# Optimization experiments

Hardware: AMD Instinct MI355X
Metric: run time of the kernel (lower is better)

Reference implementation:

```python
import jax, jax.numpy as jnp
import numpy as np
from jax import lax

B, T, D, LD, K = 128, 1024, 256, 512, 128
RD = LD + K  # 640 residual-LSTM width
PAD = 15     # (31 - 1) // 2 'same' padding for the LSA location conv


def _gru(x, h, wih, whh, bih, bhh):
    # torch.nn.GRUCell semantics, gate order [r, z, n]
    gi = x @ wih.T + bih
    gh = h @ whh.T + bhh
    ir, iz, inn = jnp.split(gi, 3, axis=-1)
    hr, hz, hn = jnp.split(gh, 3, axis=-1)
    r = jax.nn.sigmoid(ir + hr)
    z = jax.nn.sigmoid(iz + hz)
    n = jnp.tanh(inn + r * hn)
    return (1.0 - z) * n + z * h


def _lstm(x, h, c, wih, whh, bih, bhh):
    # torch.nn.LSTMCell semantics, gate order [i, f, g, o]
    g = x @ wih.T + bih + h @ whh.T + bhh
    i, f, gg, o = jnp.split(g, 4, axis=-1)
    c2 = jax.nn.sigmoid(f) * c + jax.nn.sigmoid(i) * jnp.tanh(gg)
    h2 = jax.nn.sigmoid(o) * jnp.tanh(c2)
    return h2, c2


def _forward(encoder_seq, encoder_seq_proj, prenet_in, attn_hidden, rnn1_h, rnn1_c,
             rnn2_h, rnn2_c, res_h, res_c, context_vec, cumulative, attn_prev,
             fc1_w, fc1_b, fc2_w, fc2_b, gru_wih, gru_whh, gru_bih, gru_bhh,
             conv_w, L_w, L_b, W_w, W_b, v_w, ri_w, ri_b,
             r1_wih, r1_whh, r1_bih, r1_bhh, r2_wih, r2_whh, r2_bih, r2_bhh,
             res_wih, res_whh, res_bih, res_bhh, stop_w, stop_b):
    # PreNet (dropout p = 0 in Decoder.__init__, so pure tanh-MLP)
    p = jnp.tanh(prenet_in @ fc1_w.T + fc1_b)
    prenet_out = jnp.tanh(p @ fc2_w.T + fc2_b)                     # [B, D//2]
    # Attention GRU
    attn_in = jnp.concatenate([context_vec, prenet_out], axis=-1)  # [B, D + D//2]
    attn_h = _gru(attn_in, attn_hidden, gru_wih, gru_whh, gru_bih, gru_bhh)  # [B, D]
    # LSA location-sensitive attention (cumulative/attn_prev are zeros at t=0)
    pq = (attn_h @ W_w.T + W_b)[:, None, :]                        # [B, 1, D]
    loc = jnp.stack([cumulative, attn_prev], axis=1)               # [B, 2, T]
    conv_out = lax.conv_general_dilated(loc, conv_w, (1,), [(PAD, PAD)],
                                        dimension_numbers=('NCH', 'OIH', 'NCH'))  # [B, 32, T]
    ploc = jnp.swapaxes(conv_out, 1, 2) @ L_w.T + L_b              # [B, T, D]
    u = jnp.squeeze(jnp.tanh(pq + encoder_seq_proj + ploc) @ v_w.T, -1)  # [B, T]
    sig = jax.nn.sigmoid(u)
    scores = sig / jnp.sum(sig, axis=1, keepdims=True)             # [B, T]
    cum_new = cumulative + scores
    context = jnp.einsum('bt,btd->bd', scores, encoder_seq)        # [B, D]
    # rnn_input projection + two residual LSTM cells (eval: no zoneout)
    x = jnp.concatenate([context, attn_h], axis=1) @ ri_w.T + ri_b  # [B, LD]
    h1, c1 = _lstm(x, rnn1_h, rnn1_c, r1_wih, r1_whh, r1_bih, r1_bhh)
    x = x + h1
    h2, c2 = _lstm(x, rnn2_h, rnn2_c, r2_wih, r2_whh, r2_bih, r2_bhh)
    x = x + h2
    # 4-layer residual LSTM stack on [prenet_in, x]
    res_x = jnp.concatenate([prenet_in, x], axis=1)                # [B, RD]
    hs, cs = [], []
    for i in range(4):
        hi, ci = _lstm(res_x, res_h[i], res_c[i], res_wih[i], res_whh[i], res_bih[i], res_bhh[i])
        res_x = res_x + hi
        hs.append(hi)
        cs.append(ci)
    cond = res_x                                                   # cond_features [B, RD]
    stop = jax.nn.sigmoid(cond @ stop_w.T + stop_b)                # [B, 1]
    return (cond, stop, scores, attn_h, h1, c1, h2, c2,
            jnp.stack(hs), jnp.stack(cs), context, cum_new)


def setup_inputs() -> dict:
    keys = iter(jax.random.split(jax.random.key(0), 64))
    nxt = lambda: next(keys)
    rn = lambda s: jax.random.normal(nxt(), s, jnp.float32)
    wp = lambda s: rn(s) * 0.02
    return {
        'encoder_seq': rn((B, T, D)),
        'encoder_seq_proj': rn((B, T, D)),
        'prenet_in': rn((B, K)),
        'attn_hidden': rn((B, D)),
        'rnn1_h': rn((B, LD)), 'rnn1_c': rn((B, LD)),
        'rnn2_h': rn((B, LD)), 'rnn2_c': rn((B, LD)),
        'res_h': rn((4, B, RD)), 'res_c': rn((4, B, RD)),
        'context_vec': rn((B, D)),
        'cumulative': jnp.zeros((B, T), jnp.float32),
        'attn_prev': jnp.zeros((B, T), jnp.float32),
        'fc1_w': wp((256, K)), 'fc1_b': jnp.zeros((256,), jnp.float32),
        'fc2_w': wp((D // 2, 256)), 'fc2_b': jnp.zeros((D // 2,), jnp.float32),
        'gru_wih': wp((3 * D, D + D // 2)), 'gru_whh': wp((3 * D, D)),
        'gru_bih': jnp.zeros((3 * D,), jnp.float32), 'gru_bhh': jnp.zeros((3 * D,), jnp.float32),
        'conv_w': wp((32, 2, 31)),
        'L_w': wp((D, 32)), 'L_b': jnp.zeros((D,), jnp.float32),
        'W_w': wp((D, D)), 'W_b': jnp.zeros((D,), jnp.float32),
        'v_w': wp((1, D)),
        'ri_w': wp((LD, 2 * D)), 'ri_b': jnp.zeros((LD,), jnp.float32),
        'r1_wih': wp((4 * LD, LD)), 'r1_whh': wp((4 * LD, LD)),
        'r1_bih': jnp.zeros((4 * LD,), jnp.float32), 'r1_bhh': jnp.zeros((4 * LD,), jnp.float32),
        'r2_wih': wp((4 * LD, LD)), 'r2_whh': wp((4 * LD, LD)),
        'r2_bih': jnp.zeros((4 * LD,), jnp.float32), 'r2_bhh': jnp.zeros((4 * LD,), jnp.float32),
        'res_wih': wp((4, 4 * RD, RD)), 'res_whh': wp((4, 4 * RD, RD)),
        'res_bih': jnp.zeros((4, 4 * RD), jnp.float32), 'res_bhh': jnp.zeros((4, 4 * RD), jnp.float32),
        'stop_w': wp((1, RD)), 'stop_b': jnp.zeros((1,), jnp.float32),
    }


def reference(encoder_seq, encoder_seq_proj, prenet_in, attn_hidden, rnn1_h, rnn1_c,
              rnn2_h, rnn2_c, res_h, res_c, context_vec, cumulative, attn_prev,
              fc1_w, fc1_b, fc2_w, fc2_b, gru_wih, gru_whh, gru_bih, gru_bhh,
              conv_w, L_w, L_b, W_w, W_b, v_w, ri_w, ri_b,
              r1_wih, r1_whh, r1_bih, r1_bhh, r2_wih, r2_whh, r2_bih, r2_bhh,
              res_wih, res_whh, res_bih, res_bhh, stop_w, stop_b):
    return _forward(encoder_seq, encoder_seq_proj, prenet_in, attn_hidden, rnn1_h, rnn1_c,
                    rnn2_h, rnn2_c, res_h, res_c, context_vec, cumulative, attn_prev,
                    fc1_w, fc1_b, fc2_w, fc2_b, gru_wih, gru_whh, gru_bih, gru_bhh,
                    conv_w, L_w, L_b, W_w, W_b, v_w, ri_w, ri_b,
                    r1_wih, r1_whh, r1_bih, r1_bhh, r2_wih, r2_whh, r2_bih, r2_bhh,
                    res_wih, res_whh, res_bih, res_bhh, stop_w, stop_b)
```

## Files before the change

### kernel.cpp

```cpp
#include <hip/hip_runtime.h>

#define DEV __device__ __forceinline__

typedef __attribute__((ext_vector_type(8))) short short8;
typedef __attribute__((ext_vector_type(4))) float f32x4;

DEV float fast_rcp(float x) { return __builtin_amdgcn_rcpf(x); }
DEV float sigm(float x) { return fast_rcp(1.0f + __expf(-x)); }
DEV float tanhf_fast(float x) { return 1.0f - 2.0f * fast_rcp(1.0f + __expf(2.0f * x)); }

DEV short f2bf(float f) {
    unsigned u = __float_as_uint(f);
    unsigned r = (u + 0x7FFFu + ((u >> 16) & 1u)) >> 16;
    return (short)r;
}
DEV float bf2f(short h) {
    return __uint_as_float(((unsigned)(unsigned short)h) << 16);
}
DEV void split1(float f, short& h, short& l) {
    h = f2bf(f);
    l = f2bf(f - bf2f(h));
}

__global__ __launch_bounds__(256) void convert_w_kernel(
    const float* __restrict__ p0, const float* __restrict__ p1,
    const float* __restrict__ p2, const float* __restrict__ p3,
    const float* __restrict__ p4, const float* __restrict__ p5,
    const float* __restrict__ p6, const float* __restrict__ p7,
    const float* __restrict__ p8, const float* __restrict__ p9,
    const float* __restrict__ p10, const float* __restrict__ p11,
    short* __restrict__ hi, short* __restrict__ lo)
{
    const int c1 = 8192, c2 = 16384, c3 = 90112, c4 = 139264, c5 = 155648,
              c6 = 221184, c7 = 483328, c8 = 745472, c9 = 1007616,
              c10 = 1269760, c11 = 2908160, total = 4546560;
    for (int v = blockIdx.x * 256 + threadIdx.x; v < total; v += gridDim.x * 256) {
        const float* s = p0; int base = 0;
        if (v >= c1)  { s = p1;  base = c1; }
        if (v >= c2)  { s = p2;  base = c2; }
        if (v >= c3)  { s = p3;  base = c3; }
        if (v >= c4)  { s = p4;  base = c4; }
        if (v >= c5)  { s = p5;  base = c5; }
        if (v >= c6)  { s = p6;  base = c6; }
        if (v >= c7)  { s = p7;  base = c7; }
        if (v >= c8)  { s = p8;  base = c8; }
        if (v >= c9)  { s = p9;  base = c9; }
        if (v >= c10) { s = p10; base = c10; }
        if (v >= c11) { s = p11; base = c11; }
        float4 f = ((const float4*)s)[v - base];
        short4 h, l;
        split1(f.x, h.x, l.x);
        split1(f.y, h.y, l.y);
        split1(f.z, h.z, l.z);
        split1(f.w, h.w, l.w);
        ((short4*)hi)[v] = h;
        ((short4*)lo)[v] = l;
    }
}

__global__ __launch_bounds__(256) void gemm_mfma_kernel(
    const float* __restrict__ A1, int K1,
    const short* __restrict__ W1hi, const short* __restrict__ W1lo, int ldw1,
    const float* __restrict__ A2, int K2,
    const short* __restrict__ W2hi, const short* __restrict__ W2lo, int ldw2,
    float* __restrict__ Cp, int N, int KS, int KC)
{
    const int tid = threadIdx.x;
    const int chunk = blockIdx.x % KS;
    const int n0 = (blockIdx.x / KS) * 32;
    const int kbeg = chunk * KC;
    const int w = tid >> 6, lane = tid & 63;
    const int q = lane >> 4, r = lane & 15;
    const int m_base = w * 32;

    f32x4 acc[2][2];
#pragma unroll
    for (int mt = 0; mt < 2; ++mt)
#pragma unroll
        for (int nt = 0; nt < 2; ++nt)
            acc[mt][nt] = (f32x4){0.f, 0.f, 0.f, 0.f};

    auto load_frag = [&](int kg, float4 (&a)[2][2], short8 (&bh)[2], short8 (&bl)[2]) {
        const float* A; const short *Wh, *Wl; int lda, ldw, kc;
        if (kg < K1) { A = A1; Wh = W1hi; Wl = W1lo; lda = K1; ldw = ldw1; kc = kg; }
        else         { A = A2; Wh = W2hi; Wl = W2lo; lda = K2; ldw = ldw2; kc = kg - K1; }
#pragma unroll
        for (int mt = 0; mt < 2; ++mt) {
            const float* ap = A + (size_t)(m_base + mt * 16 + r) * lda + kc + q * 8;
            a[mt][0] = *(const float4*)ap;
            a[mt][1] = *(const float4*)(ap + 4);
        }
#pragma unroll
        for (int nt = 0; nt < 2; ++nt) {
            size_t off = (size_t)(n0 + nt * 16 + r) * ldw + kc + q * 8;
            bh[nt] = *(const short8*)(Wh + off);
            bl[nt] = *(const short8*)(Wl + off);
        }
    };

    auto compute = [&](const float4 (&a)[2][2], const short8 (&bh)[2], const short8 (&bl)[2]) {
#pragma unroll
        for (int mt = 0; mt < 2; ++mt) {
            float fv[8] = {a[mt][0].x, a[mt][0].y, a[mt][0].z, a[mt][0].w,
                           a[mt][1].x, a[mt][1].y, a[mt][1].z, a[mt][1].w};
            short8 ah, al;
#pragma unroll
            for (int j = 0; j < 8; ++j) {
                short h, l;
                split1(fv[j], h, l);
                ah[j] = h; al[j] = l;
            }
#pragma unroll
            for (int nt = 0; nt < 2; ++nt) {
                acc[mt][nt] = __builtin_amdgcn_mfma_f32_16x16x32_bf16(ah, bh[nt], acc[mt][nt], 0, 0, 0);
                acc[mt][nt] = __builtin_amdgcn_mfma_f32_16x16x32_bf16(al, bh[nt], acc[mt][nt], 0, 0, 0);
                acc[mt][nt] = __builtin_amdgcn_mfma_f32_16x16x32_bf16(ah, bl[nt], acc[mt][nt], 0, 0, 0);
            }
        }
    };

    float4 a0[2][2], a1[2][2];
    short8 bh0[2], bl0[2], bh1[2], bl1[2];
    const int nsteps = KC >> 5;

    load_frag(kbeg, a0, bh0, bl0);
    for (int s = 0; s + 1 < nsteps; ++s) {
        if (s & 1) { load_frag(kbeg + (s + 1) * 32, a0, bh0, bl0); compute(a1, bh1, bl1); }
        else       { load_frag(kbeg + (s + 1) * 32, a1, bh1, bl1); compute(a0, bh0, bl0); }
    }
    if ((nsteps - 1) & 1) compute(a1, bh1, bl1);
    else                  compute(a0, bh0, bl0);

    float* Co = Cp + (size_t)chunk * 128 * N;
#pragma unroll
    for (int mt = 0; mt < 2; ++mt)
#pragma unroll
        for (int nt = 0; nt < 2; ++nt)
#pragma unroll
            for (int i = 0; i < 4; ++i)
                Co[(size_t)(m_base + mt * 16 + q * 4 + i) * N + n0 + nt * 16 + r] = acc[mt][nt][i];
}

__global__ void reduce_act_kernel(const float* __restrict__ p, int KS, int MN,
                                  const float* __restrict__ b,
                                  float* __restrict__ out, int N, int act)
{
    int idx = blockIdx.x * 256 + threadIdx.x;
    if (idx >= MN) return;
    int n = idx % N;
    float v = b ? b[n] : 0.f;
    for (int s = 0; s < KS; ++s) v += p[(size_t)s * MN + idx];
    if (act) v = tanhf_fast(v);
    out[idx] = v;
}

__global__ void gru_gate_kernel(const float* __restrict__ gi_p, int KSi,
                                const float* __restrict__ gh_p, int KSh,
                                const float* __restrict__ bih, const float* __restrict__ bhh,
                                const float* __restrict__ h, float* __restrict__ out)
{
    const size_t MN = 128 * 768;
    int m = blockIdx.x, d = threadIdx.x;
    size_t base = (size_t)m * 768 + d;
    float ir = bih[d], iz = bih[256 + d], in = bih[512 + d];
    for (int s = 0; s < KSi; ++s) {
        const float* p = gi_p + s * MN + base;
        ir += p[0]; iz += p[256]; in += p[512];
    }
    float hr = bhh[d], hz = bhh[256 + d], hn = bhh[512 + d];
    for (int s = 0; s < KSh; ++s) {
        const float* p = gh_p + s * MN + base;
        hr += p[0]; hz += p[256]; hn += p[512];
    }
    float r = sigm(ir + hr);
    float z = sigm(iz + hz);
    float n = tanhf_fast(in + r * hn);
    out[m * 256 + d] = (1.f - z) * n + z * h[m * 256 + d];
}

__global__ void lstm_gate_kernel(const float* __restrict__ gp, int KS,
                                 const float* __restrict__ bih, const float* __restrict__ bhh,
                                 const float* __restrict__ c_in,
                                 float* __restrict__ h_out, float* __restrict__ c_out,
                                 float* __restrict__ xacc, int H)
{
    int d = blockIdx.x * 256 + threadIdx.x;
    int m = blockIdx.y;
    if (d >= H) return;
    const size_t MN = (size_t)128 * 4 * H;
    size_t base = (size_t)m * 4 * H + d;
    float iv = bih[d] + bhh[d];
    float fv = bih[H + d] + bhh[H + d];
    float gv = bih[2 * H + d] + bhh[2 * H + d];
    float ov = bih[3 * H + d] + bhh[3 * H + d];
    for (int s = 0; s < KS; ++s) {
        const float* p = gp + s * MN + base;
        iv += p[0]; fv += p[H]; gv += p[2 * H]; ov += p[3 * H];
    }
    float c2 = sigm(fv) * c_in[m * H + d] + sigm(iv) * tanhf_fast(gv);
    float h2 = sigm(ov) * tanhf_fast(c2);
    h_out[m * H + d] = h2;
    c_out[m * H + d] = c2;
    if (xacc) xacc[m * H + d] += h2;
}

__global__ void lw_bf16_kernel(const float* __restrict__ Lw, short* __restrict__ LwBf)
{
    int i = blockIdx.x * 256 + threadIdx.x;
    LwBf[i] = f2bf(Lw[i]);
}

__global__ __launch_bounds__(256) void attn_u_kernel(
    const float* __restrict__ esp, const float* __restrict__ pq,
    const short* __restrict__ LwBf, const float* __restrict__ Lb,
    const float* __restrict__ vw, const float* __restrict__ cw,
    const float* __restrict__ cum, const float* __restrict__ prev,
    float* __restrict__ sig_out)
{
    const int b = blockIdx.x >> 4;
    const int t0 = (blockIdx.x & 15) << 6;
    const int tid = threadIdx.x;

    __shared__ float cum_s[94], prev_s[94];
    __shared__ float cw_s[2][32][33];
    __shared__ short conv_bf[64 * 32];
    __shared__ short lw_bf[256 * 32];
    __shared__ float pq_s[256], vw_s[256];

    if (tid < 94) {
        int ti = t0 - 15 + tid;
        cum_s[tid] = (ti >= 0 && ti < 1024) ? cum[b * 1024 + ti] : 0.f;
    } else if (tid >= 128 && tid < 222) {
        int i = tid - 128;
        int ti = t0 - 15 + i;
        prev_s[i] = (ti >= 0 && ti < 1024) ? prev[b * 1024 + ti] : 0.f;
    }
    for (int i = tid; i < 2048; i += 256) {
        int which = i >> 10, c = (i >> 5) & 31, k = i & 31;
        cw_s[which][c][k] = (k < 31) ? cw[(c * 2 + which) * 31 + k] : 0.f;
    }
    {
        const int4* src = (const int4*)LwBf;
        int4* dst = (int4*)lw_bf;
#pragma unroll
        for (int k = 0; k < 4; ++k) dst[tid + k * 256] = src[tid + k * 256];
    }
    pq_s[tid] = pq[b * 256 + tid] + Lb[tid];
    vw_s[tid] = vw[tid];
    __syncthreads();

    {
        int c = tid & 31, t8 = (tid >> 5) << 3;
        float a[8] = {0.f, 0.f, 0.f, 0.f, 0.f, 0.f, 0.f, 0.f};
        for (int k = 0; k < 31; ++k) {
            float w0 = cw_s[0][c][k], w1 = cw_s[1][c][k];
#pragma unroll
            for (int j = 0; j < 8; ++j)
                a[j] += w0 * cum_s[t8 + j + k] + w1 * prev_s[t8 + j + k];
        }
#pragma unroll
        for (int j = 0; j < 8; ++j) conv_bf[(t8 + j) * 32 + c] = f2bf(a[j]);
    }
    __syncthreads();

    const int lane = tid & 63, w = tid >> 6;
    const int q = lane >> 4, c16 = lane & 15;
    const int myt = t0 + w * 16 + c16;

    short8 bfrag = *(const short8*)&conv_bf[(w * 16 + c16) * 32 + q * 8];
    const float* er = esp + ((size_t)(b * 1024 + myt) << 8);

    float s = 0.f;
#pragma unroll
    for (int dt = 0; dt < 16; ++dt) {
        short8 afrag = *(const short8*)&lw_bf[(dt * 16 + c16) * 32 + q * 8];
        f32x4 acc = {0.f, 0.f, 0.f, 0.f};
        acc = __builtin_amdgcn_mfma_f32_16x16x32_bf16(afrag, bfrag, acc, 0, 0, 0);
        const int d0 = dt * 16 + q * 4;
        float4 e   = *(const float4*)(er + d0);
        float4 pqv = *(const float4*)&pq_s[d0];
        float4 vwv = *(const float4*)&vw_s[d0];
        s += tanhf_fast(pqv.x + e.x + acc[0]) * vwv.x;
        s += tanhf_fast(pqv.y + e.y + acc[1]) * vwv.y;
        s += tanhf_fast(pqv.z + e.z + acc[2]) * vwv.z;
        s += tanhf_fast(pqv.w + e.w + acc[3]) * vwv.w;
    }
    s += __shfl_xor(s, 16);
    s += __shfl_xor(s, 32);
    if (lane < 16)
        sig_out[b * 1024 + t0 + w * 16 + lane] = sigm(s);
}

__global__ void attn_norm_kernel(const float* __restrict__ sig, const float* __restrict__ cum,
                                 float* __restrict__ scores, float* __restrict__ cum_new,
                                 float* __restrict__ ctx)
{
    __shared__ float red[4];
    int b = blockIdx.x, tid = threadIdx.x;
    float4 sv = *(const float4*)&sig[b * 1024 + tid * 4];
    float s = sv.x + sv.y + sv.z + sv.w;
#pragma unroll
    for (int off = 1; off < 64; off <<= 1) s += __shfl_xor(s, off);
    if ((tid & 63) == 0) red[tid >> 6] = s;
    __syncthreads();
    float inv = fast_rcp(red[0] + red[1] + red[2] + red[3]);
    float4 cv = *(const float4*)&cum[b * 1024 + tid * 4];
    float4 sc = {sv.x * inv, sv.y * inv, sv.z * inv, sv.w * inv};
    *(float4*)&scores[b * 1024 + tid * 4] = sc;
    float4 cn = {cv.x + sc.x, cv.y + sc.y, cv.z + sc.z, cv.w + sc.w};
    *(float4*)&cum_new[b * 1024 + tid * 4] = cn;
    ctx[b * 256 + tid] = 0.f;
}

__global__ void attn_ctx_kernel(const float* __restrict__ scores, const float* __restrict__ es,
                                float* __restrict__ ctx)
{
    __shared__ float sc_s[128];
    int b = blockIdx.x >> 3;
    int tbase = (blockIdx.x & 7) * 128;
    int tid = threadIdx.x;
    if (tid < 128) sc_s[tid] = scores[b * 1024 + tbase + tid];
    __syncthreads();
    float a = 0.f;
    const float* ep = es + ((size_t)(b * 1024 + tbase)) * 256 + tid;
#pragma unroll 4
    for (int tt = 0; tt < 128; ++tt)
        a += sc_s[tt] * ep[(size_t)tt * 256];
    atomicAdd(&ctx[b * 256 + tid], a);
}

__global__ void build_rescat_kernel(const float* __restrict__ pre, const float* __restrict__ x,
                                    float* __restrict__ res)
{
    int idx = blockIdx.x * 256 + threadIdx.x;
    int m = idx / 640, d = idx - m * 640;
    res[idx] = (d < 128) ? pre[m * 128 + d] : x[m * 512 + d - 128];
}

__global__ void copy_kernel(const float* __restrict__ src, float* __restrict__ dst, int n)
{
    int idx = blockIdx.x * 256 + threadIdx.x;
    if (idx < n) dst[idx] = src[idx];
}

__global__ void stop_kernel(const float* __restrict__ res, const float* __restrict__ sw,
                            const float* __restrict__ sb, float* __restrict__ stop)
{
    int m = blockIdx.x, lane = threadIdx.x;
    float s = 0.f;
    for (int k = lane; k < 640; k += 64) s += res[m * 640 + k] * sw[k];
#pragma unroll
    for (int off = 1; off < 64; off <<= 1) s += __shfl_xor(s, off);
    if (lane == 0) stop[m] = sigm(s + sb[0]);
}

extern "C" void kernel_launch(void* const* d_in, const int* in_sizes, int n_in,
                              void* d_out, int out_size, void* d_ws, size_t ws_size,
                              hipStream_t stream)
{
    const float* encoder_seq      = (const float*)d_in[0];
    const float* encoder_seq_proj = (const float*)d_in[1];
    const float* prenet_in        = (const float*)d_in[2];
    const float* attn_hidden      = (const float*)d_in[3];
    const float* rnn1_h  = (const float*)d_in[4];
    const float* rnn1_c  = (const float*)d_in[5];
    const float* rnn2_h  = (const float*)d_in[6];
    const float* rnn2_c  = (const float*)d_in[7];
    const float* res_h   = (const float*)d_in[8];
    const float* res_c   = (const float*)d_in[9];
    const float* context_vec = (const float*)d_in[10];
    const float* cumulative  = (const float*)d_in[11];
    const float* attn_prev   = (const float*)d_in[12];
    const float* fc1_w = (const float*)d_in[13];
    const float* fc1_b = (const float*)d_in[14];
    const float* fc2_w = (const float*)d_in[15];
    const float* fc2_b = (const float*)d_in[16];
    const float* gru_wih = (const float*)d_in[17];
    const float* gru_whh = (const float*)d_in[18];
    const float* gru_bih = (const float*)d_in[19];
    const float* gru_bhh = (const float*)d_in[20];
    const float* conv_w = (const float*)d_in[21];
    const float* L_w = (const float*)d_in[22];
    const float* L_b = (const float*)d_in[23];
    const float* W_w = (const float*)d_in[24];
    const float* W_b = (const float*)d_in[25];
    const float* v_w = (const float*)d_in[26];
    const float* ri_w = (const float*)d_in[27];
    const float* ri_b = (const float*)d_in[28];
    const float* r1_wih = (const float*)d_in[29];
    const float* r1_whh = (const float*)d_in[30];
    const float* r1_bih = (const float*)d_in[31];
    const float* r1_bhh = (const float*)d_in[32];
    const float* r2_wih = (const float*)d_in[33];
    const float* r2_whh = (const float*)d_in[34];
    const float* r2_bih = (const float*)d_in[35];
    const float* r2_bhh = (const float*)d_in[36];
    const float* res_wih = (const float*)d_in[37];
    const float* res_whh = (const float*)d_in[38];
    const float* res_bih = (const float*)d_in[39];
    const float* res_bhh = (const float*)d_in[40];
    const float* stop_w = (const float*)d_in[41];
    const float* stop_b = (const float*)d_in[42];

    float* ws  = (float*)d_ws;
    float* out = (float*)d_out;

    const size_t OFF_P    = 0;
    const size_t OFF_POUT = 32768;
    const size_t OFF_PQ   = 49152;
    const size_t OFF_SIG  = 81920;
    const size_t OFF_X    = 212992;
    const size_t OFF_RES  = 278528;
    const size_t OFF_LWT  = 360448;
    const size_t OFF_PART = 368640;
    const size_t OFF_PARTB = OFF_PART + (size_t)12 * 128 * 768;
    const size_t OFF_WBF  = 4000000;

    const size_t WOFF_FC1 = 0,        WOFF_FC2 = 32768,   WOFF_GI = 65536,
                 WOFF_GH  = 360448,   WOFF_WW  = 557056,  WOFF_RI = 622592,
                 WOFF_R1I = 884736,   WOFF_R1H = 1933312, WOFF_R2I = 2981888,
                 WOFF_R2H = 4030464,  WOFF_RESI = 5079040, WOFF_RESH = 11632640,
                 W_TOTAL  = 18186240;
    short* WHI = (short*)(ws + OFF_WBF);
    short* WLO = WHI + W_TOTAL;

    const size_t O_COND   = 0;
    const size_t O_STOP   = 81920;
    const size_t O_SCORES = 82048;
    const size_t O_ATTNH  = 213120;
    const size_t O_H1     = 245888;
    const size_t O_C1     = 311424;
    const size_t O_H2     = 376960;
    const size_t O_C2     = 442496;
    const size_t O_HS     = 508032;
    const size_t O_CS     = 835712;
    const size_t O_CTX    = 1163392;
    const size_t O_CUM    = 1196160;

    convert_w_kernel<<<2048, 256, 0, stream>>>(
        fc1_w, fc2_w, gru_wih, gru_whh, W_w, ri_w,
        r1_wih, r1_whh, r2_wih, r2_whh, res_wih, res_whh, WHI, WLO);

    short* lwbf = (short*)(ws + OFF_LWT);
    lw_bf16_kernel<<<32, 256, 0, stream>>>(L_w, lwbf);

    gemm_mfma_kernel<<<8 * 4, 256, 0, stream>>>(
        prenet_in, 128, WHI + WOFF_FC1, WLO + WOFF_FC1, 128,
        nullptr, 0, nullptr, nullptr, 0,
        ws + OFF_PART, 256, 4, 32);
    reduce_act_kernel<<<128, 256, 0, stream>>>(ws + OFF_PART, 4, 128 * 256, fc1_b,
                                               ws + OFF_P, 256, 1);
    gemm_mfma_kernel<<<4 * 8, 256, 0, stream>>>(
        ws + OFF_P, 256, WHI + WOFF_FC2, WLO + WOFF_FC2, 256,
        nullptr, 0, nullptr, nullptr, 0,
        ws + OFF_PART, 128, 8, 32);
    reduce_act_kernel<<<64, 256, 0, stream>>>(ws + OFF_PART, 8, 128 * 128, fc2_b,
                                              ws + OFF_POUT, 128, 1);

    gemm_mfma_kernel<<<24 * 12, 256, 0, stream>>>(
        context_vec, 256, WHI + WOFF_GI, WLO + WOFF_GI, 384,
        ws + OFF_POUT, 128, WHI + WOFF_GI + 256, WLO + WOFF_GI + 256, 384,
        ws + OFF_PART, 768, 12, 32);
    gemm_mfma_kernel<<<24 * 8, 256, 0, stream>>>(
        attn_hidden, 256, WHI + WOFF_GH, WLO + WOFF_GH, 256,
        nullptr, 0, nullptr, nullptr, 0,
        ws + OFF_PARTB, 768, 8, 32);
    gru_gate_kernel<<<128, 256, 0, stream>>>(ws + OFF_PART, 12, ws + OFF_PARTB, 8,
                                             gru_bih, gru_bhh, attn_hidden, out + O_ATTNH);

    gemm_mfma_kernel<<<8 * 8, 256, 0, stream>>>(
        out + O_ATTNH, 256, WHI + WOFF_WW, WLO + WOFF_WW, 256,
        nullptr, 0, nullptr, nullptr, 0,
        ws + OFF_PART, 256, 8, 32);
    reduce_act_kernel<<<128, 256, 0, stream>>>(ws + OFF_PART, 8, 128 * 256, W_b,
                                               ws + OFF_PQ, 256, 0);

    attn_u_kernel<<<2048, 256, 0, stream>>>(encoder_seq_proj, ws + OFF_PQ, lwbf,
                                            L_b, v_w, conv_w, cumulative, attn_prev,
                                            ws + OFF_SIG);
    attn_norm_kernel<<<128, 256, 0, stream>>>(ws + OFF_SIG, cumulative,
                                              out + O_SCORES, out + O_CUM, out + O_CTX);
    attn_ctx_kernel<<<1024, 256, 0, stream>>>(out + O_SCORES, encoder_seq, out + O_CTX);

    gemm_mfma_kernel<<<16 * 8, 256, 0, stream>>>(
        out + O_CTX, 256, WHI + WOFF_RI, WLO + WOFF_RI, 512,
        out + O_ATTNH, 256, WHI + WOFF_RI + 256, WLO + WOFF_RI + 256, 512,
        ws + OFF_PART, 512, 8, 64);
    reduce_act_kernel<<<256, 256, 0, stream>>>(ws + OFF_PART, 8, 128 * 512, ri_b,
                                               ws + OFF_X, 512, 0);

    gemm_mfma_kernel<<<64 * 8, 256, 0, stream>>>(
        ws + OFF_X, 512, WHI + WOFF_R1I, WLO + WOFF_R1I, 512,
        rnn1_h, 512, WHI + WOFF_R1H, WLO + WOFF_R1H, 512,
        ws + OFF_PART, 2048, 8, 128);
    lstm_gate_kernel<<<dim3(2, 128), 256, 0, stream>>>(ws + OFF_PART, 8, r1_bih, r1_bhh,
                                                       rnn1_c, out + O_H1, out + O_C1,
                                                       ws + OFF_X, 512);
    gemm_mfma_kernel<<<64 * 8, 256, 0, stream>>>(
        ws + OFF_X, 512, WHI + WOFF_R2I, WLO + WOFF_R2I, 512,
        rnn2_h, 512, WHI + WOFF_R2H, WLO + WOFF_R2H, 512,
        ws + OFF_PART, 2048, 8, 128);
    lstm_gate_kernel<<<dim3(2, 128), 256, 0, stream>>>(ws + OFF_PART, 8, r2_bih, r2_bhh,
                                                       rnn2_c, out + O_H2, out + O_C2,
                                                       ws + OFF_X, 512);

    build_rescat_kernel<<<320, 256, 0, stream>>>(prenet_in, ws + OFF_X, ws + OFF_RES);

    for (int i = 0; i < 4; ++i) {
        const short* wih_hi = WHI + WOFF_RESI + (size_t)i * 2560 * 640;
        const short* wih_lo = WLO + WOFF_RESI + (size_t)i * 2560 * 640;
        const short* whh_hi = WHI + WOFF_RESH + (size_t)i * 2560 * 640;
        const short* whh_lo = WLO + WOFF_RESH + (size_t)i * 2560 * 640;
        gemm_mfma_kernel<<<80 * 8, 256, 0, stream>>>(
            ws + OFF_RES, 640, wih_hi, wih_lo, 640,
            res_h + (size_t)i * 81920, 640, whh_hi, whh_lo, 640,
            ws + OFF_PART, 2560, 8, 160);
        lstm_gate_kernel<<<dim3(3, 128), 256, 0, stream>>>(ws + OFF_PART, 8,
                                                           res_bih + (size_t)i * 2560,
                                                           res_bhh + (size_t)i * 2560,
                                                           res_c + (size_t)i * 81920,
                                                           out + O_HS + (size_t)i * 81920,
                                                           out + O_CS + (size_t)i * 81920,
                                                           ws + OFF_RES, 640);
    }

    copy_kernel<<<320, 256, 0, stream>>>(ws + OFF_RES, out + O_COND, 128 * 640);
    stop_kernel<<<128, 64, 0, stream>>>(ws + OFF_RES, stop_w, stop_b, out + O_STOP);
}
```

Measured before the change: 634.2 us.

## Fuse split-K GEMMs with gate epilogues into single-kernel GRU/LSTM/FC layers

Replaces the split-K GEMM plus separate reduce/gate kernels with fused kernels. Each block computes the input-weight and hidden-weight products in two wave groups, combines them through shared memory, and applies bias, activation and the GRU/LSTM gate math directly. Residual buffers are ping-ponged so no in-place race occurs, and the final conditioning copy is written from the last LSTM epilogue. This removes partial-sum round trips through global memory and many kernel launches, at the cost of far fewer blocks per launch (64–80) and a longer serial K loop per wave.

New measurement: 771.3 us. 21.6% more time.

```diff
diff --git a/kernel.cpp b/kernel.cpp
--- a/kernel.cpp
+++ b/kernel.cpp
@@ -20,6 +20,18 @@
 DEV void split1(float f, short& h, short& l) {
     h = f2bf(f);
     l = f2bf(f - bf2f(h));
+}
+DEV void split8(const float4& x0, const float4& x1, short8& h, short8& l) {
+    float fv[8] = {x0.x, x0.y, x0.z, x0.w, x1.x, x1.y, x1.z, x1.w};
+#pragma unroll
+    for (int j = 0; j < 8; ++j) { short hh, ll; split1(fv[j], hh, ll); h[j] = hh; l[j] = ll; }
+}
+#define MFMA16 __builtin_amdgcn_mfma_f32_16x16x32_bf16
+DEV f32x4 mfma3(const short8& ah, const short8& al, const short8& bh, const short8& bl, f32x4 acc) {
+    acc = MFMA16(ah, bh, acc, 0, 0, 0);
+    acc = MFMA16(al, bh, acc, 0, 0, 0);
+    acc = MFMA16(ah, bl, acc, 0, 0, 0);
+    return acc;
 }
 
 __global__ __launch_bounds__(256) void convert_w_kernel(
@@ -58,150 +70,224 @@
     }
 }
 
-__global__ __launch_bounds__(256) void gemm_mfma_kernel(
-    const float* __restrict__ A1, int K1,
-    const short* __restrict__ W1hi, const short* __restrict__ W1lo, int ldw1,
-    const float* __restrict__ A2, int K2,
-    const short* __restrict__ W2hi, const short* __restrict__ W2lo, int ldw2,
-    float* __restrict__ Cp, int N, int KS, int KC)
-{
-    const int tid = threadIdx.x;
-    const int chunk = blockIdx.x % KS;
-    const int n0 = (blockIdx.x / KS) * 32;
-    const int kbeg = chunk * KC;
-    const int w = tid >> 6, lane = tid & 63;
-    const int q = lane >> 4, r = lane & 15;
-    const int m_base = w * 32;
-
-    f32x4 acc[2][2];
-#pragma unroll
-    for (int mt = 0; mt < 2; ++mt)
-#pragma unroll
-        for (int nt = 0; nt < 2; ++nt)
-            acc[mt][nt] = (f32x4){0.f, 0.f, 0.f, 0.f};
-
-    auto load_frag = [&](int kg, float4 (&a)[2][2], short8 (&bh)[2], short8 (&bl)[2]) {
-        const float* A; const short *Wh, *Wl; int lda, ldw, kc;
-        if (kg < K1) { A = A1; Wh = W1hi; Wl = W1lo; lda = K1; ldw = ldw1; kc = kg; }
-        else         { A = A2; Wh = W2hi; Wl = W2lo; lda = K2; ldw = ldw2; kc = kg - K1; }
-#pragma unroll
-        for (int mt = 0; mt < 2; ++mt) {
-            const float* ap = A + (size_t)(m_base + mt * 16 + r) * lda + kc + q * 8;
-            a[mt][0] = *(const float4*)ap;
-            a[mt][1] = *(const float4*)(ap + 4);
+__global__ __launch_bounds__(512) void fc_fused_kernel(
+    const float* __restrict__ A1, int lda1,
+    const short* __restrict__ W1hi, const short* __restrict__ W1lo, int ldw1, int K1,
+    const float* __restrict__ A2, int lda2,
+    const short* __restrict__ W2hi, const short* __restrict__ W2lo, int ldw2, int K2,
+    const float* __restrict__ bias, float* __restrict__ out, int N, int act)
+{
+    __shared__ float red[4][64][17];
+    const int tid = threadIdx.x, w = tid >> 6, kk = w >> 2, mtw = w & 3;
+    const int lane = tid & 63, q = lane >> 4, r = lane & 15;
+    const int rowbase = blockIdx.y * 64 + mtw * 16, n0 = blockIdx.x * 16;
+
+    const float* A = kk ? A2 : A1;
+    const int lda = kk ? lda2 : lda1, K = kk ? K2 : K1, ldw = kk ? ldw2 : ldw1;
+    const short* Whi = kk ? W2hi : W1hi;
+    const short* Wlo = kk ? W2lo : W1lo;
+    const float* ar = A + (size_t)(rowbase + r) * lda;
+    const short* wh = Whi + (size_t)(n0 + r) * ldw;
+    const short* wl = Wlo + (size_t)(n0 + r) * ldw;
+
+    f32x4 acc = {0.f, 0.f, 0.f, 0.f};
+    float4 a0A, a1A, a0B, a1B;
+    short8 bhA, blA, bhB, blB;
+
+    auto ld = [&](int k0, float4& x0, float4& x1, short8& bh, short8& bl) {
+        x0 = *(const float4*)(ar + k0 + q * 8);
+        x1 = *(const float4*)(ar + k0 + q * 8 + 4);
+        bh = *(const short8*)(wh + k0 + q * 8);
+        bl = *(const short8*)(wl + k0 + q * 8);
+    };
+    auto cp = [&](const float4& x0, const float4& x1, const short8& bh, const short8& bl) {
+        short8 ah, al;
+        split8(x0, x1, ah, al);
+        acc = mfma3(ah, al, bh, bl, acc);
+    };
+
+    const int ns = K >> 5;
+    ld(0, a0A, a1A, bhA, blA);
+    for (int s = 0; s + 1 < ns; ++s) {
+        if (s & 1) { ld((s + 1) << 5, a0A, a1A, bhA, blA); cp(a0B, a1B, bhB, blB); }
+        else       { ld((s + 1) << 5, a0B, a1B, bhB, blB); cp(a0A, a1A, bhA, blA); }
+    }
+    if ((ns - 1) & 1) cp(a0B, a1B, bhB, blB);
+    else              cp(a0A, a1A, bhA, blA);
+
+    if (kk) {
+#pragma unroll
+        for (int i = 0; i < 4; ++i) red[mtw][lane][i] = acc[i];
+    }
+    __syncthreads();
+    if (!kk) {
+        float b = bias ? bias[n0 + r] : 0.f;
+#pragma unroll
+        for (int i = 0; i < 4; ++i) {
+            float v = acc[i] + red[mtw][lane][i] + b;
+            if (act) v = tanhf_fast(v);
+            out[(size_t)(rowbase + q * 4 + i) * N + n0 + r] = v;
         }
-#pragma unroll
-        for (int nt = 0; nt < 2; ++nt) {
-            size_t off = (size_t)(n0 + nt * 16 + r) * ldw + kc + q * 8;
-            bh[nt] = *(const short8*)(Wh + off);
-            bl[nt] = *(const short8*)(Wl + off);
+    }
+}
+
+__global__ __launch_bounds__(512) void gru_fused_kernel(
+    const float* __restrict__ ctx, const float* __restrict__ pout,
+    const short* __restrict__ Wihi, const short* __restrict__ Wilo,
+    const short* __restrict__ Whhi, const short* __restrict__ Whlo,
+    const float* __restrict__ bih, const float* __restrict__ bhh,
+    const float* __restrict__ h_old, float* __restrict__ h_new)
+{
+    __shared__ float red[4][64][13];
+    const int tid = threadIdx.x, w = tid >> 6, kk = w >> 2, mtw = w & 3;
+    const int lane = tid & 63, q = lane >> 4, r = lane & 15;
+    const int rowbase = blockIdx.y * 64 + mtw * 16, d0 = blockIdx.x * 16, col = d0 + r;
+
+    const float* A1 = kk ? h_old : ctx;
+    const int K1 = 256, Ktot = kk ? 256 : 384, ldw = kk ? 256 : 384;
+    const short* Whi = kk ? Whhi : Wihi;
+    const short* Wlo = kk ? Whlo : Wilo;
+
+    const short* wh[3]; const short* wl[3];
+#pragma unroll
+    for (int g = 0; g < 3; ++g) {
+        size_t ro = (size_t)(g * 256 + col) * ldw;
+        wh[g] = Whi + ro; wl[g] = Wlo + ro;
+    }
+    const float* ar1 = A1 + (size_t)(rowbase + r) * 256;
+    const float* ar2 = pout + (size_t)(rowbase + r) * 128;
+
+    f32x4 acc[3] = {{0,0,0,0},{0,0,0,0},{0,0,0,0}};
+    float4 a0A, a1A, a0B, a1B;
+    short8 bhA[3], blA[3], bhB[3], blB[3];
+
+    auto ld = [&](int kv, float4& x0, float4& x1, short8 (&bh)[3], short8 (&bl)[3]) {
+        const float* ap = (kv < K1) ? (ar1 + kv) : (ar2 + kv - K1);
+        x0 = *(const float4*)(ap + q * 8);
+        x1 = *(const float4*)(ap + q * 8 + 4);
+#pragma unroll
+        for (int g = 0; g < 3; ++g) {
+            bh[g] = *(const short8*)(wh[g] + kv + q * 8);
+            bl[g] = *(const short8*)(wl[g] + kv + q * 8);
         }
     };
-
-    auto compute = [&](const float4 (&a)[2][2], const short8 (&bh)[2], const short8 (&bl)[2]) {
-#pragma unroll
-        for (int mt = 0; mt < 2; ++mt) {
-            float fv[8] = {a[mt][0].x, a[mt][0].y, a[mt][0].z, a[mt][0].w,
-                           a[mt][1].x, a[mt][1].y, a[mt][1].z, a[mt][1].w};
-            short8 ah, al;
-#pragma unroll
-            for (int j = 0; j < 8; ++j) {
-                short h, l;
-                split1(fv[j], h, l);
-                ah[j] = h; al[j] = l;
-            }
-#pragma unroll
-            for (int nt = 0; nt < 2; ++nt) {
-                acc[mt][nt] = __builtin_amdgcn_mfma_f32_16x16x32_bf16(ah, bh[nt], acc[mt][nt], 0, 0, 0);
-                acc[mt][nt] = __builtin_amdgcn_mfma_f32_16x16x32_bf16(al, bh[nt], acc[mt][nt], 0, 0, 0);
-                acc[mt][nt] = __builtin_amdgcn_mfma_f32_16x16x32_bf16(ah, bl[nt], acc[mt][nt], 0, 0, 0);
-            }
+    auto cp = [&](const float4& x0, const float4& x1, const short8 (&bh)[3], const short8 (&bl)[3]) {
+        short8 ah, al;
+        split8(x0, x1, ah, al);
+#pragma unroll
+        for (int g = 0; g < 3; ++g) acc[g] = mfma3(ah, al, bh[g], bl[g], acc[g]);
+    };
+
+    const int ns = Ktot >> 5;
+    ld(0, a0A, a1A, bhA, blA);
+    for (int s = 0; s + 1 < ns; ++s) {
+        if (s & 1) { ld((s + 1) << 5, a0A, a1A, bhA, blA); cp(a0B, a1B, bhB, blB); }
+        else       { ld((s + 1) << 5, a0B, a1B, bhB, blB); cp(a0A, a1A, bhA, blA); }
+    }
+    if ((ns - 1) & 1) cp(a0B, a1B, bhB, blB);
+    else              cp(a0A, a1A, bhA, blA);
+
+    if (kk) {
+#pragma unroll
+        for (int g = 0; g < 3; ++g)
+#pragma unroll
+            for (int i = 0; i < 4; ++i) red[mtw][lane][g * 4 + i] = acc[g][i];
+    }
+    __syncthreads();
+    if (!kk) {
+#pragma unroll
+        for (int i = 0; i < 4; ++i) {
+            int row = rowbase + q * 4 + i;
+            float ir = acc[0][i] + bih[col],       hr = red[mtw][lane][0 + i] + bhh[col];
+            float iz = acc[1][i] + bih[256 + col], hz = red[mtw][lane][4 + i] + bhh[256 + col];
+            float in = acc[2][i] + bih[512 + col], hn = red[mtw][lane][8 + i] + bhh[512 + col];
+            float rr = sigm(ir + hr), zz = sigm(iz + hz);
+            float nn = tanhf_fast(in + rr * hn);
+            float ho = h_old[(size_t)row * 256 + col];
+            h_new[(size_t)row * 256 + col] = (1.f - zz) * nn + zz * ho;
+        }
+    }
+}
+
+__global__ __launch_bounds__(512) void lstm_fused_kernel(
+    const float* __restrict__ Ax, const short* __restrict__ Wxhi, const short* __restrict__ Wxlo,
+    const float* __restrict__ Ah, const short* __restrict__ Whhi, const short* __restrict__ Whlo,
+    int K, int H,
+    const float* __restrict__ bih, const float* __restrict__ bhh,
+    const float* __restrict__ c_in, float* __restrict__ h_out, float* __restrict__ c_out,
+    const float* __restrict__ x_old, float* __restrict__ x_new, float* __restrict__ cond)
+{
+    __shared__ float red[4][64][17];
+    const int tid = threadIdx.x, w = tid >> 6, kk = w >> 2, mtw = w & 3;
+    const int lane = tid & 63, q = lane >> 4, r = lane & 15;
+    const int rowbase = blockIdx.y * 64 + mtw * 16, d0 = blockIdx.x * 16, col = d0 + r;
+
+    const float* A = kk ? Ah : Ax;
+    const short* Whi = kk ? Whhi : Wxhi;
+    const short* Wlo = kk ? Whlo : Wxlo;
+
+    const short* wh[4]; const short* wl[4];
+#pragma unroll
+    for (int g = 0; g < 4; ++g) {
+        size_t ro = (size_t)(g * H + col) * K;
+        wh[g] = Whi + ro; wl[g] = Wlo + ro;
+    }
+    const float* ar = A + (size_t)(rowbase + r) * K;
+
+    f32x4 acc[4] = {{0,0,0,0},{0,0,0,0},{0,0,0,0},{0,0,0,0}};
+    float4 a0A, a1A, a0B, a1B;
+    short8 bhA[4], blA[4], bhB[4], blB[4];
+
+    auto ld = [&](int k0, float4& x0, float4& x1, short8 (&bh)[4], short8 (&bl)[4]) {
+        x0 = *(const float4*)(ar + k0 + q * 8);
+        x1 = *(const float4*)(ar + k0 + q * 8 + 4);
+#pragma unroll
+        for (int g = 0; g < 4; ++g) {
+            bh[g] = *(const short8*)(wh[g] + k0 + q * 8);
+            bl[g] = *(const short8*)(wl[g] + k0 + q * 8);
         }
     };
-
-    float4 a0[2][2], a1[2][2];
-    short8 bh0[2], bl0[2], bh1[2], bl1[2];
-    const int nsteps = KC >> 5;
-
-    load_frag(kbeg, a0, bh0, bl0);
-    for (int s = 0; s + 1 < nsteps; ++s) {
-        if (s & 1) { load_frag(kbeg + (s + 1) * 32, a0, bh0, bl0); compute(a1, bh1, bl1); }
-        else       { load_frag(kbeg + (s + 1) * 32, a1, bh1, bl1); compute(a0, bh0, bl0); }
-    }
-    if ((nsteps - 1) & 1) compute(a1, bh1, bl1);
-    else                  compute(a0, bh0, bl0);
-
-    float* Co = Cp + (size_t)chunk * 128 * N;
-#pragma unroll
-    for (int mt = 0; mt < 2; ++mt)
-#pragma unroll
-        for (int nt = 0; nt < 2; ++nt)
-#pragma unroll
-            for (int i = 0; i < 4; ++i)
-                Co[(size_t)(m_base + mt * 16 + q * 4 + i) * N + n0 + nt * 16 + r] = acc[mt][nt][i];
-}
-
-__global__ void reduce_act_kernel(const float* __restrict__ p, int KS, int MN,
-                                  const float* __restrict__ b,
-                                  float* __restrict__ out, int N, int act)
-{
-    int idx = blockIdx.x * 256 + threadIdx.x;
-    if (idx >= MN) return;
-    int n = idx % N;
-    float v = b ? b[n] : 0.f;
-    for (int s = 0; s < KS; ++s) v += p[(size_t)s * MN + idx];
-    if (act) v = tanhf_fast(v);
-    out[idx] = v;
-}
-
-__global__ void gru_gate_kernel(const float* __restrict__ gi_p, int KSi,
-                                const float* __restrict__ gh_p, int KSh,
-                                const float* __restrict__ bih, const float* __restrict__ bhh,
-                                const float* __restrict__ h, float* __restrict__ out)
-{
-    const size_t MN = 128 * 768;
-    int m = blockIdx.x, d = threadIdx.x;
-    size_t base = (size_t)m * 768 + d;
-    float ir = bih[d], iz = bih[256 + d], in = bih[512 + d];
-    for (int s = 0; s < KSi; ++s) {
-        const float* p = gi_p + s * MN + base;
-        ir += p[0]; iz += p[256]; in += p[512];
-    }
-    float hr = bhh[d], hz = bhh[256 + d], hn = bhh[512 + d];
-    for (int s = 0; s < KSh; ++s) {
-        const float* p = gh_p + s * MN + base;
-        hr += p[0]; hz += p[256]; hn += p[512];
-    }
-    float r = sigm(ir + hr);
-    float z = sigm(iz + hz);
-    float n = tanhf_fast(in + r * hn);
-    out[m * 256 + d] = (1.f - z) * n + z * h[m * 256 + d];
-}
-
-__global__ void lstm_gate_kernel(const float* __restrict__ gp, int KS,
-                                 const float* __restrict__ bih, const float* __restrict__ bhh,
-                                 const float* __restrict__ c_in,
-                                 float* __restrict__ h_out, float* __restrict__ c_out,
-                                 float* __restrict__ xacc, int H)
-{
-    int d = blockIdx.x * 256 + threadIdx.x;
-    int m = blockIdx.y;
-    if (d >= H) return;
-    const size_t MN = (size_t)128 * 4 * H;
-    size_t base = (size_t)m * 4 * H + d;
-    float iv = bih[d] + bhh[d];
-    float fv = bih[H + d] + bhh[H + d];
-    float gv = bih[2 * H + d] + bhh[2 * H + d];
-    float ov = bih[3 * H + d] + bhh[3 * H + d];
-    for (int s = 0; s < KS; ++s) {
-        const float* p = gp + s * MN + base;
-        iv += p[0]; fv += p[H]; gv += p[2 * H]; ov += p[3 * H];
-    }
-    float c2 = sigm(fv) * c_in[m * H + d] + sigm(iv) * tanhf_fast(gv);
-    float h2 = sigm(ov) * tanhf_fast(c2);
-    h_out[m * H + d] = h2;
-    c_out[m * H + d] = c2;
-    if (xacc) xacc[m * H + d] += h2;
+    auto cp = [&](const float4& x0, const float4& x1, const short8 (&bh)[4], const short8 (&bl)[4]) {
+        short8 ah, al;
+        split8(x0, x1, ah, al);
+#pragma unroll
+        for (int g = 0; g < 4; ++g) acc[g] = mfma3(ah, al, bh[g], bl[g], acc[g]);
+    };
+
+    const int ns = K >> 5;
+    ld(0, a0A, a1A, bhA, blA);
+    for (int s = 0; s + 1 < ns; ++s) {
+        if (s & 1) { ld((s + 1) << 5, a0A, a1A, bhA, blA); cp(a0B, a1B, bhB, blB); }
+        else       { ld((s + 1) << 5, a0B, a1B, bhB, blB); cp(a0A, a1A, bhA, blA); }
+    }
+    if ((ns - 1) & 1) cp(a0B, a1B, bhB, blB);
+    else              cp(a0A, a1A, bhA, blA);
+
+    if (kk) {
+#pragma unroll
+        for (int g = 0; g < 4; ++g)
+#pragma unroll
+            for (int i = 0; i < 4; ++i) red[mtw][lane][g * 4 + i] = acc[g][i];
+    }
+    __syncthreads();
+    if (!kk) {
+#pragma unroll
+        for (int i = 0; i < 4; ++i) {
+            int row = rowbase + q * 4 + i;
+            float iv = acc[0][i] + red[mtw][lane][0 + i]  + bih[col] + bhh[col];
+            float fv = acc[1][i] + red[mtw][lane][4 + i]  + bih[H + col] + bhh[H + col];
+            float gv = acc[2][i] + red[mtw][lane][8 + i]  + bih[2 * H + col] + bhh[2 * H + col];
+            float ov = acc[3][i] + red[mtw][lane][12 + i] + bih[3 * H + col] + bhh[3 * H + col];
+            size_t o = (size_t)row * H + col;
+            float c2 = sigm(fv) * c_in[o] + sigm(iv) * tanhf_fast(gv);
+            float h2 = sigm(ov) * tanhf_fast(c2);
+            h_out[o] = h2;
+            c_out[o] = c2;
+            float xn = x_old[o] + h2;
+            x_new[o] = xn;
+            if (cond) cond[o] = xn;
+        }
+    }
 }
 
 __global__ void lw_bf16_kernel(const float* __restrict__ Lw, short* __restrict__ LwBf)
@@ -275,7 +361,7 @@
     for (int dt = 0; dt < 16; ++dt) {
         short8 afrag = *(const short8*)&lw_bf[(dt * 16 + c16) * 32 + q * 8];
         f32x4 acc = {0.f, 0.f, 0.f, 0.f};
-        acc = __builtin_amdgcn_mfma_f32_16x16x32_bf16(afrag, bfrag, acc, 0, 0, 0);
+        acc = MFMA16(afrag, bfrag, acc, 0, 0, 0);
         const int d0 = dt * 16 + q * 4;
         float4 e   = *(const float4*)(er + d0);
         float4 pqv = *(const float4*)&pq_s[d0];
@@ -335,12 +421,6 @@
     int idx = blockIdx.x * 256 + threadIdx.x;
     int m = idx / 640, d = idx - m * 640;
     res[idx] = (d < 128) ? pre[m * 128 + d] : x[m * 512 + d - 128];
-}
-
-__global__ void copy_kernel(const float* __restrict__ src, float* __restrict__ dst, int n)
-{
-    int idx = blockIdx.x * 256 + threadIdx.x;
-    if (idx < n) dst[idx] = src[idx];
 }
 
 __global__ void stop_kernel(const float* __restrict__ res, const float* __restrict__ sw,
@@ -410,11 +490,12 @@
     const size_t OFF_PQ   = 49152;
     const size_t OFF_SIG  = 81920;
     const size_t OFF_X    = 212992;
-    const size_t OFF_RES  = 278528;
-    const size_t OFF_LWT  = 360448;
-    const size_t OFF_PART = 368640;
-    const size_t OFF_PARTB = OFF_PART + (size_t)12 * 128 * 768;
-    const size_t OFF_WBF  = 4000000;
+    const size_t OFF_XB   = 278528;
+    const size_t OFF_XC   = 344064;
+    const size_t OFF_R0   = 409600;
+    const size_t OFF_R1   = 491520;
+    const size_t OFF_LWT  = 573440;
+    const size_t OFF_WBF  = 577536;
 
     const size_t WOFF_FC1 = 0,        WOFF_FC2 = 32768,   WOFF_GI = 65536,
                  WOFF_GH  = 360448,   WOFF_WW  = 557056,  WOFF_RI = 622592,
@@ -444,36 +525,24 @@
     short* lwbf = (short*)(ws + OFF_LWT);
     lw_bf16_kernel<<<32, 256, 0, stream>>>(L_w, lwbf);
 
-    gemm_mfma_kernel<<<8 * 4, 256, 0, stream>>>(
-        prenet_in, 128, WHI + WOFF_FC1, WLO + WOFF_FC1, 128,
-        nullptr, 0, nullptr, nullptr, 0,
-        ws + OFF_PART, 256, 4, 32);
-    reduce_act_kernel<<<128, 256, 0, stream>>>(ws + OFF_PART, 4, 128 * 256, fc1_b,
-                                               ws + OFF_P, 256, 1);
-    gemm_mfma_kernel<<<4 * 8, 256, 0, stream>>>(
-        ws + OFF_P, 256, WHI + WOFF_FC2, WLO + WOFF_FC2, 256,
-        nullptr, 0, nullptr, nullptr, 0,
-        ws + OFF_PART, 128, 8, 32);
-    reduce_act_kernel<<<64, 256, 0, stream>>>(ws + OFF_PART, 8, 128 * 128, fc2_b,
-                                              ws + OFF_POUT, 128, 1);
-
-    gemm_mfma_kernel<<<24 * 12, 256, 0, stream>>>(
-        context_vec, 256, WHI + WOFF_GI, WLO + WOFF_GI, 384,
-        ws + OFF_POUT, 128, WHI + WOFF_GI + 256, WLO + WOFF_GI + 256, 384,
-        ws + OFF_PART, 768, 12, 32);
-    gemm_mfma_kernel<<<24 * 8, 256, 0, stream>>>(
-        attn_hidden, 256, WHI + WOFF_GH, WLO + WOFF_GH, 256,
-        nullptr, 0, nullptr, nullptr, 0,
-        ws + OFF_PARTB, 768, 8, 32);
-    gru_gate_kernel<<<128, 256, 0, stream>>>(ws + OFF_PART, 12, ws + OFF_PARTB, 8,
-                                             gru_bih, gru_bhh, attn_hidden, out + O_ATTNH);
-
-    gemm_mfma_kernel<<<8 * 8, 256, 0, stream>>>(
-        out + O_ATTNH, 256, WHI + WOFF_WW, WLO + WOFF_WW, 256,
-        nullptr, 0, nullptr, nullptr, 0,
-        ws + OFF_PART, 256, 8, 32);
-    reduce_act_kernel<<<128, 256, 0, stream>>>(ws + OFF_PART, 8, 128 * 256, W_b,
-                                               ws + OFF_PQ, 256, 0);
+    fc_fused_kernel<<<dim3(16, 2), 512, 0, stream>>>(
+        prenet_in, 128, WHI + WOFF_FC1, WLO + WOFF_FC1, 128, 64,
+        prenet_in + 64, 128, WHI + WOFF_FC1 + 64, WLO + WOFF_FC1 + 64, 128, 64,
+        fc1_b, ws + OFF_P, 256, 1);
+    fc_fused_kernel<<<dim3(8, 2), 512, 0, stream>>>(
+        ws + OFF_P, 256, WHI + WOFF_FC2, WLO + WOFF_FC2, 256, 128,
+        ws + OFF_P + 128, 256, WHI + WOFF_FC2 + 128, WLO + WOFF_FC2 + 128, 256, 128,
+        fc2_b, ws + OFF_POUT, 128, 1);
+
+    gru_fused_kernel<<<dim3(16, 2), 512, 0, stream>>>(
+        context_vec, ws + OFF_POUT,
+        WHI + WOFF_GI, WLO + WOFF_GI, WHI + WOFF_GH, WLO + WOFF_GH,
+        gru_bih, gru_bhh, attn_hidden, out + O_ATTNH);
+
+    fc_fused_kernel<<<dim3(16, 2), 512, 0, stream>>>(
+        out + O_ATTNH, 256, WHI + WOFF_WW, WLO + WOFF_WW, 256, 128,
+        out + O_ATTNH + 128, 256, WHI + WOFF_WW + 128, WLO + WOFF_WW + 128, 256, 128,
+        W_b, ws + OFF_PQ, 256, 0);
 
     attn_u_kernel<<<2048, 256, 0, stream>>>(encoder_seq_proj, ws + OFF_PQ, lwbf,
                                             L_b, v_w, conv_w, cumulative, attn_prev,
@@ -482,48 +551,36 @@
                                               out + O_SCORES, out + O_CUM, out + O_CTX);
     attn_ctx_kernel<<<1024, 256, 0, stream>>>(out + O_SCORES, encoder_seq, out + O_CTX);
 
-    gemm_mfma_kernel<<<16 * 8, 256, 0, stream>>>(
-        out + O_CTX, 256, WHI + WOFF_RI, WLO + WOFF_RI, 512,
-        out + O_ATTNH, 256, WHI + WOFF_RI + 256, WLO + WOFF_RI + 256, 512,
-        ws + OFF_PART, 512, 8, 64);
-    reduce_act_kernel<<<256, 256, 0, stream>>>(ws + OFF_PART, 8, 128 * 512, ri_b,
-                                               ws + OFF_X, 512, 0);
-
-    gemm_mfma_kernel<<<64 * 8, 256, 0, stream>>>(
-        ws + OFF_X, 512, WHI + WOFF_R1I, WLO + WOFF_R1I, 512,
-        rnn1_h, 512, WHI + WOFF_R1H, WLO + WOFF_R1H, 512,
-        ws + OFF_PART, 2048, 8, 128);
-    lstm_gate_kernel<<<dim3(2, 128), 256, 0, stream>>>(ws + OFF_PART, 8, r1_bih, r1_bhh,
-                                                       rnn1_c, out + O_H1, out + O_C1,
-                                                       ws + OFF_X, 512);
-    gemm_mfma_kernel<<<64 * 8, 256, 0, stream>>>(
-        ws + OFF_X, 512, WHI + WOFF_R2I, WLO + WOFF_R2I, 512,
-        rnn2_h, 512, WHI + WOFF_R2H, WLO + WOFF_R2H, 512,
-        ws + OFF_PART, 2048, 8, 128);
-    lstm_gate_kernel<<<dim3(2, 128), 256, 0, stream>>>(ws + OFF_PART, 8, r2_bih, r2_bhh,
-                                                       rnn2_c, out + O_H2, out + O_C2,
-                                                       ws + OFF_X, 512);
-
-    build_rescat_kernel<<<320, 256, 0, stream>>>(prenet_in, ws + OFF_X, ws + OFF_RES);
+    fc_fused_kernel<<<dim3(32, 2), 512, 0, stream>>>(
+        out + O_CTX, 256, WHI + WOFF_RI, WLO + WOFF_RI, 512, 256,
+        out + O_ATTNH, 256, WHI + WOFF_RI + 256, WLO + WOFF_RI + 256, 512, 256,
+        ri_b, ws + OFF_X, 512, 0);
+
+    lstm_fused_kernel<<<dim3(32, 2), 512, 0, stream>>>(
+        ws + OFF_X, WHI + WOFF_R1I, WLO + WOFF_R1I,
+        rnn1_h, WHI + WOFF_R1H, WLO + WOFF_R1H,
+        512, 512, r1_bih, r1_bhh, rnn1_c, out + O_H1, out + O_C1,
+        ws + OFF_X, ws + OFF_XB, nullptr);
+    lstm_fused_kernel<<<dim3(32, 2), 512, 0, stream>>>(
+        ws + OFF_XB, WHI + WOFF_R2I, WLO + WOFF_R2I,
+        rnn2_h, WHI + WOFF_R2H, WLO + WOFF_R2H,
+        512, 512, r2_bih, r2_bhh, rnn2_c, out + O_H2, out + O_C2,
+        ws + OFF_XB, ws + OFF_XC, nullptr);
+
+    build_rescat_kernel<<<320, 256, 0, stream>>>(prenet_in, ws + OFF_XC, ws + OFF_R0);
 
     for (int i = 0; i < 4; ++i) {
-        const short* wih_hi = WHI + WOFF_RESI + (size_t)i * 2560 * 640;
-        const short* wih_lo = WLO + WOFF_RESI + (size_t)i * 2560 * 640;
-        const short* whh_hi = WHI + WOFF_RESH + (size_t)i * 2560 * 640;
-        const short* whh_lo = WLO + WOFF_RESH + (size_t)i * 2560 * 640;
-        gemm_mfma_kernel<<<80 * 8, 256, 0, stream>>>(
-            ws + OFF_RES, 640, wih_hi, wih_lo, 640,
-            res_h + (size_t)i * 81920, 640, whh_hi, whh_lo, 640,
-            ws + OFF_PART, 2560, 8, 160);
-        lstm_gate_kernel<<<dim3(3, 128), 256, 0, stream>>>(ws + OFF_PART, 8,
-                                                           res_bih + (size_t)i * 2560,
-                                                           res_bhh + (size_t)i * 2560,
-                                                           res_c + (size_t)i * 81920,
-                                                           out + O_HS + (size_t)i * 81920,
-                                                           out + O_CS + (size_t)i * 81920,
-                                                           ws + OFF_RES, 640);
-    }
-
-    copy_kernel<<<320, 256, 0, stream>>>(ws + OFF_RES, out + O_COND, 128 * 640);
-    stop_kernel<<<128, 64, 0, stream>>>(ws + OFF_RES, stop_w, stop_b, out + O_STOP);
-}
+        const float* rcur = ws + ((i & 1) ? OFF_R1 : OFF_R0);
+        float* rnxt = ws + ((i & 1) ? OFF_R0 : OFF_R1);
+        lstm_fused_kernel<<<dim3(40, 2), 512, 0, stream>>>(
+            rcur, WHI + WOFF_RESI + (size_t)i * 2560 * 640, WLO + WOFF_RESI + (size_t)i * 2560 * 640,
+            res_h + (size_t)i * 81920, WHI + WOFF_RESH + (size_t)i * 2560 * 640, WLO + WOFF_RESH + (size_t)i * 2560 * 640,
+            640, 640,
+            res_bih + (size_t)i * 2560, res_bhh + (size_t)i * 2560,
+            res_c + (size_t)i * 81920,
+            out + O_HS + (size_t)i * 81920, out + O_CS + (size_t)i * 81920,
+            rcur, rnxt, (i == 3) ? (out + O_COND) : nullptr);
+    }
+
+    stop_kernel<<<128, 64, 0, stream>>>(ws + OFF_R0, stop_w, stop_b, out + O_STOP);
+}
```
